# Optimization experiments

Measured on AMD Instinct MI355X. Metric: run time of the kernel, lower is better.

## Reference

```python
import jax, jax.numpy as jnp
import numpy as np

VOCAB = 100277
EMBED = 32
B, S = 8, 512


def setup_inputs() -> dict:
    key = jax.random.key(0)
    k1, k2, k3, k4 = jax.random.split(key, 4)
    input_seq = jax.random.randint(k1, (B, S), 0, VOCAB, dtype=jnp.int64)
    predictions = jax.random.randint(k2, (B, S), 0, VOCAB, dtype=jnp.int64)
    emb = jax.random.normal(k3, (VOCAB, EMBED), dtype=jnp.float32)
    # torch Linear default init scale ~ 1/sqrt(fan_in); keep simple gaussian scaled
    W = jax.random.normal(k4, (VOCAB, EMBED), dtype=jnp.float32) * (1.0 / np.sqrt(EMBED))
    b = jnp.zeros((VOCAB,), dtype=jnp.float32)
    return {"input_seq": input_seq, "predictions": predictions, "emb": emb, "W": W, "b": b}


def reference(input_seq, predictions, emb, W, b):
    # embedding lookup: [B,S,E]
    embeds = emb[input_seq]
    # linear projection to vocab: [B,S,V]
    logits = jnp.einsum('bse,ve->bsv', embeds, W) + b
    n, v = B * S, VOCAB
    logits_flat = logits.reshape(n, v)
    targets = predictions.reshape(n)
    # mean cross-entropy (stable log_softmax, single pass)
    logp = jax.nn.log_softmax(logits_flat, axis=-1)
    nll = -jnp.take_along_axis(logp, targets[:, None], axis=-1)[:, 0]
    loss = jnp.mean(nll)
    return (logits_flat, loss)
```

## Files before the change

### kernel.cpp

```cpp
#include <hip/hip_runtime.h>
#include <cstddef>
#include <cstdint>


using f32x4 = __attribute__((ext_vector_type(4))) float;
using f16x8 = __attribute__((ext_vector_type(8))) _Float16;

constexpr int N_ROWS  = 4096;
constexpr int ROWS_PB = 16;
constexpr int NBLK    = N_ROWS / ROWS_PB;
constexpr int WIN     = 2048;
constexpr int NWIN    = 49;
constexpr int TPB     = 1024;
constexpr int WAVES   = 16;
constexpr int V_TILES = NWIN * (WIN / 16);
constexpr int TSTR    = 2052;

constexpr size_t RS_OFF = 0;
constexpr size_t EF_OFF = 64 * 1024;
constexpr size_t EF_BYTES = (size_t)NBLK * 64 * 16;
constexpr size_t WF_OFF = EF_OFF + EF_BYTES;

static __device__ __forceinline__ uint4 pack8h(const float* f) {
    unsigned short u[8];
#pragma unroll
    for (int i = 0; i < 8; ++i) {
        _Float16 h = (_Float16)f[i];
        u[i] = __builtin_bit_cast(unsigned short, h);
    }
    uint4 r;
    r.x = (unsigned)u[0] | ((unsigned)u[1] << 16);
    r.y = (unsigned)u[2] | ((unsigned)u[3] << 16);
    r.z = (unsigned)u[4] | ((unsigned)u[5] << 16);
    r.w = (unsigned)u[6] | ((unsigned)u[7] << 16);
    return r;
}

__global__ __launch_bounds__(256) void prep_wfrag(
    const float* __restrict__ W, uint4* __restrict__ Wf, int V)
{
    const int g    = blockIdx.x * 256 + threadIdx.x;
    const int lane = g & 63;
    const int tile = g >> 6;
    int col = tile * 16 + (lane & 15);
    if (col >= V) col = V - 1;
    const int k0 = (lane >> 4) * 8;
    const float* wp = W + (size_t)col * 32 + k0;
    float f[8];
    *reinterpret_cast<float4*>(f)     = *reinterpret_cast<const float4*>(wp);
    *reinterpret_cast<float4*>(f + 4) = *reinterpret_cast<const float4*>(wp + 4);
    Wf[g] = pack8h(f);
}

__global__ __launch_bounds__(256) void prep_efrag(
    const int* __restrict__ seq, const float* __restrict__ emb,
    uint4* __restrict__ Ef)
{
    const int g    = blockIdx.x * 256 + threadIdx.x;
    const int lane = g & 63;
    const int c    = g >> 6;
    const int row  = c * 16 + (lane & 15);
    const int k0   = (lane >> 4) * 8;
    const int idx  = seq[row];
    const float* ep = emb + (size_t)idx * 32 + k0;
    float f[8];
    *reinterpret_cast<float4*>(f)     = *reinterpret_cast<const float4*>(ep);
    *reinterpret_cast<float4*>(f + 4) = *reinterpret_cast<const float4*>(ep + 4);
    Ef[g] = pack8h(f);
}

__global__ __launch_bounds__(TPB) void bigram_main(
    const uint4* __restrict__ Wf,
    const float* __restrict__ bias,
    const uint4* __restrict__ Ef,
    float*       __restrict__ logits,
    float*       __restrict__ rowsum,
    int V)
{
    __shared__ float buf[ROWS_PB][TSTR];
    __shared__ float lsum[WAVES][ROWS_PB];

    const int tid  = threadIdx.x;
    const int lane = tid & 63;
    const int wid  = tid >> 6;
    const int lgrp = lane >> 4;
    const int lcol = lane & 15;
    const int b    = blockIdx.x;

    const f16x8 E = __builtin_bit_cast(f16x8, Ef[(size_t)b * 64 + lane]);
    const int wcol = wid * 128;
    float rs = 0.f;

    uint4 Wc[8];
#pragma unroll
    for (int t = 0; t < 8; ++t)
        Wc[t] = Wf[(size_t)(wid * 8 + t) * 64 + lane];

    for (int s = 0; s < NWIN; ++s) {
        const int  cbase = s * WIN;
        const bool last  = (s == NWIN - 1);

        const int sp = (s + 1 < NWIN) ? s + 1 : s;
        uint4 Wn[8];
#pragma unroll
        for (int t = 0; t < 8; ++t)
            Wn[t] = Wf[(size_t)(sp * (WIN / 16) + wid * 8 + t) * 64 + lane];

#pragma unroll
        for (int t = 0; t < 8; ++t) {
            const f32x4 z = {0.f, 0.f, 0.f, 0.f};
            f32x4 acc = __builtin_amdgcn_mfma_f32_16x16x32_f16(
                __builtin_bit_cast(f16x8, Wc[t]), E, z, 0, 0, 0);
            const int c0 = cbase + wcol + t * 16 + lgrp * 4;
            f32x4 x;
            if (!last) {
                const float4 b4 = *reinterpret_cast<const float4*>(bias + c0);
                x = acc + f32x4{b4.x, b4.y, b4.z, b4.w};
                rs += __expf(x[0]) + __expf(x[1]) + __expf(x[2]) + __expf(x[3]);
            } else {
#pragma unroll
                for (int j = 0; j < 4; ++j) {
                    const int c = c0 + j;
                    x[j] = acc[j] + bias[c < V ? c : V - 1];
                    if (c < V) rs += __expf(x[j]);
                }
            }
            *reinterpret_cast<f32x4*>(&buf[lcol][wcol + t * 16 + lgrp * 4]) = x;
        }
        __syncthreads();

        {
            const int n = b * ROWS_PB + wid;
            float* dst = logits + (size_t)n * V + cbase;
#pragma unroll
            for (int i = 0; i < 8; ++i) {
                const int colL = i * 256 + lane * 4;
                const f32x4 v = *reinterpret_cast<const f32x4*>(&buf[wid][colL]);
                if (!last) {
                    __builtin_nontemporal_store(v, reinterpret_cast<f32x4*>(dst + colL));
                } else {
                    const int cg = cbase + colL;
                    if (cg + 3 < V) {
                        __builtin_nontemporal_store(v, reinterpret_cast<f32x4*>(dst + colL));
                    } else {
#pragma unroll
                        for (int j = 0; j < 4; ++j)
                            if (cg + j < V)
                                __builtin_nontemporal_store(v[j], dst + colL + j);
                    }
                }
            }
        }
        __syncthreads();

#pragma unroll
        for (int t = 0; t < 8; ++t) Wc[t] = Wn[t];
    }

    rs += __shfl_xor(rs, 16, 64);
    rs += __shfl_xor(rs, 32, 64);
    if (lane < 16) lsum[wid][lane] = rs;
    __syncthreads();
    if (tid < ROWS_PB) {
        float t = 0.f;
#pragma unroll
        for (int w = 0; w < WAVES; ++w) t += lsum[w][tid];
        rowsum[b * ROWS_PB + tid] = t;
    }
}

__global__ void bigram_loss(
    const int*   __restrict__ seq,
    const int*   __restrict__ pred,
    const float* __restrict__ emb,
    const float* __restrict__ W,
    const float* __restrict__ bias,
    const float* __restrict__ rowsum,
    float*       __restrict__ loss,
    int N)
{
    const int tid = threadIdx.x;
    float local = 0.f;
    for (int n = blockIdx.x * blockDim.x + tid; n < N; n += gridDim.x * blockDim.x) {
        const int r = seq[n], t = pred[n];
        const float4* e4 = reinterpret_cast<const float4*>(emb + (size_t)r * 32);
        const float4* w4 = reinterpret_cast<const float4*>(W + (size_t)t * 32);
        float d = bias[t];
#pragma unroll
        for (int i = 0; i < 8; ++i) {
            const float4 e = e4[i], w = w4[i];
            d += e.x * w.x + e.y * w.y + e.z * w.z + e.w * w.w;
        }
        local += __logf(rowsum[n]) - d;
    }
#pragma unroll
    for (int off = 32; off >= 1; off >>= 1) local += __shfl_xor(local, off, 64);
    __shared__ float r4[4];
    if ((tid & 63) == 0) r4[tid >> 6] = local;
    __syncthreads();
    if (tid == 0) {
        const float s = r4[0] + r4[1] + r4[2] + r4[3];
        atomicAdd(loss, s / (float)N);
    }
}

extern "C" void kernel_launch(void* const* d_in, const int* in_sizes, int n_in,
                              void* d_out, int out_size, void* d_ws, size_t ws_size,
                              hipStream_t stream)
{
    const int*   seq  = (const int*)d_in[0];
    const int*   pred = (const int*)d_in[1];
    const float* emb  = (const float*)d_in[2];
    const float* W    = (const float*)d_in[3];
    const float* bias = (const float*)d_in[4];

    const int N = in_sizes[0];
    const int V = in_sizes[4];

    float* logits = (float*)d_out;
    float* loss   = logits + (size_t)N * V;

    char*  ws     = (char*)d_ws;
    float* rowsum = (float*)(ws + RS_OFF);
    uint4* Ef     = (uint4*)(ws + EF_OFF);
    uint4* Wf     = (uint4*)(ws + WF_OFF);

    hipMemsetAsync((void*)loss, 0, sizeof(float), stream);

    hipLaunchKernelGGL(prep_wfrag, dim3(V_TILES * 64 / 256), dim3(256), 0, stream,
                       W, Wf, V);
    hipLaunchKernelGGL(prep_efrag, dim3(NBLK * 64 / 256), dim3(256), 0, stream,
                       seq, emb, Ef);

    hipLaunchKernelGGL(bigram_main, dim3(NBLK), dim3(TPB), 0, stream,
                       Wf, bias, Ef, logits, rowsum, V);

    hipLaunchKernelGGL(bigram_loss, dim3(16), dim3(256), 0, stream,
                       seq, pred, emb, W, bias, rowsum, loss, N);
}
```

Before: 423.9 us.

## Halve vocab window, prefetch bias, fold bias into MFMA, use raw barriers

Shrinks the per-iteration vocab window from 2048 to 1024 columns, which halves the LDS staging buffer and the per-wave tile count, so the kernel may fit more blocks per CU. Bias values are now prefetched one window ahead together with the W fragments and passed as the MFMA accumulator input, which removes the separate bias add. The __syncthreads calls are replaced with an explicit lgkmcnt wait, s_barrier and sched_barrier, so outstanding global stores are not waited on before each barrier. The trade-off is twice as many loop iterations and barriers.

```diff
diff --git a/kernel.cpp b/kernel.cpp
--- a/kernel.cpp
+++ b/kernel.cpp
@@ -9,12 +9,13 @@
 constexpr int N_ROWS  = 4096;
 constexpr int ROWS_PB = 16;
 constexpr int NBLK    = N_ROWS / ROWS_PB;
-constexpr int WIN     = 2048;
-constexpr int NWIN    = 49;
+constexpr int WIN     = 1024;
+constexpr int NWIN    = 98;
 constexpr int TPB     = 1024;
 constexpr int WAVES   = 16;
+constexpr int TILES   = 4;
 constexpr int V_TILES = NWIN * (WIN / 16);
-constexpr int TSTR    = 2052;
+constexpr int TSTR    = 1028;
 
 constexpr size_t RS_OFF = 0;
 constexpr size_t EF_OFF = 64 * 1024;
@@ -88,52 +89,68 @@
     const int b    = blockIdx.x;
 
     const f16x8 E = __builtin_bit_cast(f16x8, Ef[(size_t)b * 64 + lane]);
-    const int wcol = wid * 128;
+    const int wcol = wid * (TILES * 16);
     float rs = 0.f;
 
-    uint4 Wc[8];
-#pragma unroll
-    for (int t = 0; t < 8; ++t)
-        Wc[t] = Wf[(size_t)(wid * 8 + t) * 64 + lane];
+    uint4 Wc[TILES]; f32x4 Bc[TILES];
+#pragma unroll
+    for (int t = 0; t < TILES; ++t) {
+        Wc[t] = Wf[(size_t)(wid * TILES + t) * 64 + lane];
+        const float4 b4 = *reinterpret_cast<const float4*>(
+            bias + wcol + t * 16 + lgrp * 4);
+        Bc[t] = f32x4{b4.x, b4.y, b4.z, b4.w};
+    }
 
     for (int s = 0; s < NWIN; ++s) {
         const int  cbase = s * WIN;
         const bool last  = (s == NWIN - 1);
 
-        const int sp = (s + 1 < NWIN) ? s + 1 : s;
-        uint4 Wn[8];
-#pragma unroll
-        for (int t = 0; t < 8; ++t)
-            Wn[t] = Wf[(size_t)(sp * (WIN / 16) + wid * 8 + t) * 64 + lane];
-
-#pragma unroll
-        for (int t = 0; t < 8; ++t) {
-            const f32x4 z = {0.f, 0.f, 0.f, 0.f};
-            f32x4 acc = __builtin_amdgcn_mfma_f32_16x16x32_f16(
-                __builtin_bit_cast(f16x8, Wc[t]), E, z, 0, 0, 0);
-            const int c0 = cbase + wcol + t * 16 + lgrp * 4;
-            f32x4 x;
-            if (!last) {
+        const int  sp    = (s + 1 < NWIN) ? s + 1 : s;
+        const bool ptail = (sp == NWIN - 1);
+        uint4 Wn[TILES]; f32x4 Bn[TILES];
+#pragma unroll
+        for (int t = 0; t < TILES; ++t)
+            Wn[t] = Wf[(size_t)(sp * (WIN / 16) + wid * TILES + t) * 64 + lane];
+#pragma unroll
+        for (int t = 0; t < TILES; ++t) {
+            const int c0 = sp * WIN + wcol + t * 16 + lgrp * 4;
+            if (!ptail) {
                 const float4 b4 = *reinterpret_cast<const float4*>(bias + c0);
-                x = acc + f32x4{b4.x, b4.y, b4.z, b4.w};
-                rs += __expf(x[0]) + __expf(x[1]) + __expf(x[2]) + __expf(x[3]);
+                Bn[t] = f32x4{b4.x, b4.y, b4.z, b4.w};
             } else {
 #pragma unroll
                 for (int j = 0; j < 4; ++j) {
                     const int c = c0 + j;
-                    x[j] = acc[j] + bias[c < V ? c : V - 1];
-                    if (c < V) rs += __expf(x[j]);
+                    Bn[t][j] = bias[c < V ? c : V - 1];
                 }
             }
-            *reinterpret_cast<f32x4*>(&buf[lcol][wcol + t * 16 + lgrp * 4]) = x;
-        }
-        __syncthreads();
+        }
+
+#pragma unroll
+        for (int t = 0; t < TILES; ++t) {
+            const f32x4 acc = __builtin_amdgcn_mfma_f32_16x16x32_f16(
+                __builtin_bit_cast(f16x8, Wc[t]), E, Bc[t], 0, 0, 0);
+            if (!last) {
+                rs += __expf(acc[0]) + __expf(acc[1]) +
+                      __expf(acc[2]) + __expf(acc[3]);
+            } else {
+                const int c0 = cbase + wcol + t * 16 + lgrp * 4;
+#pragma unroll
+                for (int j = 0; j < 4; ++j)
+                    if (c0 + j < V) rs += __expf(acc[j]);
+            }
+            *reinterpret_cast<f32x4*>(&buf[lcol][wcol + t * 16 + lgrp * 4]) = acc;
+        }
+
+        asm volatile("s_waitcnt lgkmcnt(0)" ::: "memory");
+        __builtin_amdgcn_s_barrier();
+        __builtin_amdgcn_sched_barrier(0);
 
         {
             const int n = b * ROWS_PB + wid;
             float* dst = logits + (size_t)n * V + cbase;
 #pragma unroll
-            for (int i = 0; i < 8; ++i) {
+            for (int i = 0; i < 4; ++i) {
                 const int colL = i * 256 + lane * 4;
                 const f32x4 v = *reinterpret_cast<const f32x4*>(&buf[wid][colL]);
                 if (!last) {
@@ -151,15 +168,18 @@
                 }
             }
         }
-        __syncthreads();
-
-#pragma unroll
-        for (int t = 0; t < 8; ++t) Wc[t] = Wn[t];
+
+        asm volatile("s_waitcnt lgkmcnt(0)" ::: "memory");
+        __builtin_amdgcn_s_barrier();
+        __builtin_amdgcn_sched_barrier(0);
+
+#pragma unroll
+        for (int t = 0; t < TILES; ++t) { Wc[t] = Wn[t]; Bc[t] = Bn[t]; }
     }
 
     rs += __shfl_xor(rs, 16, 64);
     rs += __shfl_xor(rs, 32, 64);
-    if (lane < 16) lsum[wid][lane] = rs;
+    if (lane < 16) lsum[wid][lcol] = rs;
     __syncthreads();
     if (tid < ROWS_PB) {
         float t = 0.f;
```

After: 428.3 us. Within noise of the previous version (+1.0%).
